# Performance work log

Hardware: AMD Instinct MI355X
Metric: run time of the kernel (lower is better)

The kernel has to match this reference:

```python
import jax, jax.numpy as jnp
import numpy as np

DT = 0.01
T, D_IN, D_STATE = 262144, 64, 128

def setup_inputs() -> dict:
    key = jax.random.key(0)
    k1, k2, k3, k4 = jax.random.split(key, 4)
    U = jax.random.normal(k1, (T, D_IN), dtype=jnp.float32)
    A_log = jax.random.normal(k2, (D_STATE,), dtype=jnp.float32) * 0.1 - 1.0
    B = jax.random.normal(k3, (D_STATE, D_IN), dtype=jnp.float32) * 0.1
    C = jax.random.normal(k4, (D_IN, D_STATE), dtype=jnp.float32) * 0.1
    Dm = jnp.zeros((D_IN, D_IN), dtype=jnp.float32)
    h0 = jnp.zeros((D_STATE,), dtype=jnp.float32)
    return {"U": U, "A_log": A_log, "B": B, "C": C, "D": Dm, "h0": h0}

def reference(U, A_log, B, C, D, h0):
    # Discretized diagonal transition: A_disc = exp(A_log * dt)
    A_d = jnp.exp(A_log * DT)  # (d_state,)
    Bu = U @ B.T               # (T, d_state), precompute all input injections
    Du = U @ D.T               # (T, d_input)

    def step(h, bu):
        h_new = A_d * h + bu
        return h_new, h_new

    h_final, H = jax.lax.scan(step, h0, Bu)  # H: (T, d_state)
    Y = H @ C.T + Du                          # (T, d_input)
    return Y, h_final
```

## Files before the change

### kernel.cpp

```cpp
#include <hip/hip_runtime.h>


#define TT   262144
#define DIN  64
#define DS   128
#define DTC  0.01f
#define L    128
#define NG   (TT / L)
#define SEGL 32
#define NSEG (NG / SEGL)

typedef short  s8v  __attribute__((ext_vector_type(8)));
typedef float  f4v  __attribute__((ext_vector_type(4)));

__device__ __forceinline__ unsigned short f2bf(float f) {
    unsigned u = __float_as_uint(f);
    u += 0x7fffu + ((u >> 16) & 1u);
    return (unsigned short)(u >> 16);
}

__device__ __forceinline__ s8v pack8(float4 a, float4 b) {
    union { unsigned short u[8]; s8v v; } r;
    r.u[0] = f2bf(a.x); r.u[1] = f2bf(a.y); r.u[2] = f2bf(a.z); r.u[3] = f2bf(a.w);
    r.u[4] = f2bf(b.x); r.u[5] = f2bf(b.y); r.u[6] = f2bf(b.z); r.u[7] = f2bf(b.w);
    return r.v;
}

__device__ __forceinline__ int swl(int lane) {
    int q = lane >> 4, m = lane & 15;
    return (q << 4) | (m ^ (q << 2));
}

__device__ __forceinline__ s8v load_bfrag(const float* __restrict__ M,
                                          int row, int k0, int ld) {
    const float4* p = (const float4*)(M + row * ld + k0);
    return pack8(p[0], p[1]);
}

__device__ __forceinline__ void stage_U(const float* __restrict__ Ug,
                                        unsigned short* __restrict__ sA,
                                        int tid) {
    #pragma unroll
    for (int u = tid; u < (L / 16) * 8 * 16; u += 512) {
        int t = u >> 3, oct = u & 7;
        const float4* gp = (const float4*)(Ug + t * 64 + oct * 8);
        float4 x = gp[0], y = gp[1];
        int mt = t >> 4, ks = oct >> 2, q = oct & 3, m = t & 15;
        int slot = (mt * 2 + ks) * 64 + ((q << 4) | (m ^ (q << 2)));
        *(s8v*)&sA[slot * 8] = pack8(x, y);
    }
}

__global__ __launch_bounds__(512) void ssm_k1(
    const float* __restrict__ U, const float* __restrict__ Alog,
    const float* __restrict__ B, float* __restrict__ agg,
    float* __restrict__ segAgg)
{
    __shared__ __align__(16) unsigned short sA[8 * 2 * 64 * 8];
    __shared__ __align__(16) float sBu[64 * 132];
    const int g    = blockIdx.x;
    const int tid  = threadIdx.x;
    const int lane = tid & 63;
    const int w    = tid >> 6;
    const int q    = lane >> 4, m = lane & 15;

    stage_U(U + (size_t)g * L * DIN, sA, tid);

    s8v Bf[2];
    #pragma unroll
    for (int ks = 0; ks < 2; ++ks)
        Bf[ks] = load_bfrag(B, 16 * w + m, ks * 32 + q * 8, DIN);

    float a_s = 0.f, hreg = 0.f;
    if (tid < DS) a_s = __expf(Alog[tid] * DTC);
    __syncthreads();

    #pragma unroll
    for (int hh = 0; hh < 2; ++hh) {
        f4v acc[4];
        #pragma unroll
        for (int mtl = 0; mtl < 4; ++mtl) {
            acc[mtl] = (f4v){0.f, 0.f, 0.f, 0.f};
            const int mt = hh * 4 + mtl;
            #pragma unroll
            for (int ks = 0; ks < 2; ++ks) {
                s8v af = *(const s8v*)&sA[((mt * 2 + ks) * 64 + swl(lane)) * 8];
                acc[mtl] = __builtin_amdgcn_mfma_f32_16x16x32_bf16(af, Bf[ks], acc[mtl], 0, 0, 0);
            }
        }
        #pragma unroll
        for (int mtl = 0; mtl < 4; ++mtl)
            #pragma unroll
            for (int r = 0; r < 4; ++r)
                sBu[(mtl * 16 + q * 4 + r) * 132 + 16 * w + m] = acc[mtl][r];
        __syncthreads();

        if (tid < DS) {
            #pragma unroll
            for (int r = 0; r < 64; ++r)
                hreg = fmaf(a_s, hreg, sBu[r * 132 + tid]);
        }
        __syncthreads();
    }

    if (tid < DS) {
        agg[(size_t)g * DS + tid] = hreg;
        float wgt = __expf(Alog[tid] * (DTC * L) * (float)(SEGL - 1 - (g & (SEGL - 1))));
        atomicAdd(&segAgg[(g >> 5) * DS + tid], hreg * wgt);
    }
}

__global__ void ssm_k2(const float* __restrict__ Alog, const float* __restrict__ h0,
                       const float* __restrict__ segAgg, float* __restrict__ segCarry,
                       float* __restrict__ hfin)
{
    const int s = threadIdx.x;
    const float aSeg = __expf(Alog[s] * (DTC * L * SEGL));
    float c = h0[s];
    #pragma unroll 4
    for (int sg = 0; sg < NSEG; ++sg) {
        segCarry[sg * DS + s] = c;
        c = fmaf(aSeg, c, segAgg[sg * DS + s]);
    }
    hfin[s] = c;
}

__global__ __launch_bounds__(512) void ssm_k3(
    const float* __restrict__ U, const float* __restrict__ Alog,
    const float* __restrict__ B, const float* __restrict__ C,
    const float* __restrict__ Dm, const float* __restrict__ agg,
    const float* __restrict__ segCarry, float* __restrict__ Y)
{
    __shared__ __align__(16) unsigned short sA[8 * 2 * 64 * 8];
    __shared__ __align__(16) float sBu[64 * 132];
    __shared__ __align__(16) unsigned short sH[4 * 4 * 64 * 8];
    const int g    = blockIdx.x;
    const int tid  = threadIdx.x;
    const int lane = tid & 63;
    const int w    = tid >> 6;
    const int q    = lane >> 4, m = lane & 15;

    stage_U(U + (size_t)g * L * DIN, sA, tid);

    s8v Bf[2], Cf[4], Df[2];
    #pragma unroll
    for (int ks = 0; ks < 2; ++ks)
        Bf[ks] = load_bfrag(B, 16 * w + m, ks * 32 + q * 8, DIN);
    const int iC = 16 * (w & 3) + m;
    #pragma unroll
    for (int ks = 0; ks < 4; ++ks)
        Cf[ks] = load_bfrag(C, iC, ks * 32 + q * 8, DS);
    #pragma unroll
    for (int ks = 0; ks < 2; ++ks)
        Df[ks] = load_bfrag(Dm, iC, ks * 32 + q * 8, DIN);

    float a_s = 0.f, hreg = 0.f;
    if (tid < DS) {
        a_s = __expf(Alog[tid] * DTC);
        const float aL = __expf(Alog[tid] * (DTC * L));
        float c0 = segCarry[(g >> 5) * DS + tid];
        for (int c = g & ~(SEGL - 1); c < g; ++c)
            c0 = fmaf(aL, c0, agg[(size_t)c * DS + tid]);
        hreg = c0;
    }
    __syncthreads();

    #pragma unroll
    for (int hh = 0; hh < 2; ++hh) {
        f4v acc[4];
        #pragma unroll
        for (int mtl = 0; mtl < 4; ++mtl) {
            acc[mtl] = (f4v){0.f, 0.f, 0.f, 0.f};
            const int mt = hh * 4 + mtl;
            #pragma unroll
            for (int ks = 0; ks < 2; ++ks) {
                s8v af = *(const s8v*)&sA[((mt * 2 + ks) * 64 + swl(lane)) * 8];
                acc[mtl] = __builtin_amdgcn_mfma_f32_16x16x32_bf16(af, Bf[ks], acc[mtl], 0, 0, 0);
            }
        }
        #pragma unroll
        for (int mtl = 0; mtl < 4; ++mtl)
            #pragma unroll
            for (int r = 0; r < 4; ++r)
                sBu[(mtl * 16 + q * 4 + r) * 132 + 16 * w + m] = acc[mtl][r];
        __syncthreads();

        if (tid < DS) {
            #pragma unroll
            for (int r = 0; r < 64; ++r) {
                hreg = fmaf(a_s, hreg, sBu[r * 132 + tid]);
                sBu[r * 132 + tid] = hreg;
            }
        }
        __syncthreads();

        #pragma unroll
        for (int u = tid; u < 1024; u += 512) {
            int lp = u & 63, ks4 = (u >> 6) & 3, mth = (u >> 8) & 3;
            int qq = (lp >> 4) & 3, mm = lp & 15;
            int t = mth * 16 + mm, s0 = ks4 * 32 + qq * 8;
            const float4* hp = (const float4*)&sBu[t * 132 + s0];
            int slot = (mth * 4 + ks4) * 64 + ((qq << 4) | (mm ^ (qq << 2)));
            *(s8v*)&sH[slot * 8] = pack8(hp[0], hp[1]);
        }
        __syncthreads();

        const int mm2 = w >> 2;
        #pragma unroll
        for (int ti = 0; ti < 2; ++ti) {
            const int mtl = mm2 * 2 + ti;
            f4v acc2 = (f4v){0.f, 0.f, 0.f, 0.f};
            #pragma unroll
            for (int ks = 0; ks < 4; ++ks) {
                s8v ah = *(const s8v*)&sH[((mtl * 4 + ks) * 64 + swl(lane)) * 8];
                acc2 = __builtin_amdgcn_mfma_f32_16x16x32_bf16(ah, Cf[ks], acc2, 0, 0, 0);
            }
            #pragma unroll
            for (int ks = 0; ks < 2; ++ks) {
                s8v au = *(const s8v*)&sA[(((hh * 4 + mtl) * 2 + ks) * 64 + swl(lane)) * 8];
                acc2 = __builtin_amdgcn_mfma_f32_16x16x32_bf16(au, Df[ks], acc2, 0, 0, 0);
            }
            const size_t tb = (size_t)g * L + hh * 64 + mtl * 16 + q * 4;
            #pragma unroll
            for (int r = 0; r < 4; ++r)
                Y[(tb + r) * DIN + iC] = acc2[r];
        }
        __syncthreads();
    }
}

extern "C" void kernel_launch(void* const* d_in, const int* in_sizes, int n_in,
                              void* d_out, int out_size, void* d_ws, size_t ws_size,
                              hipStream_t stream)
{
    const float* U    = (const float*)d_in[0];
    const float* Alog = (const float*)d_in[1];
    const float* B    = (const float*)d_in[2];
    const float* C    = (const float*)d_in[3];
    const float* Dm   = (const float*)d_in[4];
    const float* h0   = (const float*)d_in[5];

    float* out  = (float*)d_out;
    float* Yp   = out;
    float* hfin = out + (size_t)TT * DIN;

    float* agg      = (float*)d_ws;
    float* segAgg   = agg + (size_t)NG * DS;
    float* segCarry = segAgg + (size_t)NSEG * DS;

    hipMemsetAsync(segAgg, 0, (size_t)NSEG * DS * sizeof(float), stream);
    ssm_k1<<<NG, 512, 0, stream>>>(U, Alog, B, agg, segAgg);
    ssm_k2<<<1, DS, 0, stream>>>(Alog, h0, segAgg, segCarry, hfin);
    ssm_k3<<<NG, 512, 0, stream>>>(U, Alog, B, C, Dm, agg, segCarry, Yp);
}
```

Measured before the change: 210.8 us.

## Replace serial chunk scan in pass 1 with decay-weighted MFMA reduction

Pass 1 no longer runs a 128-thread sequential recurrence over the chunk. Each lane now weights its MFMA outputs by the decay power a^(L-1-t) and reduces across lanes with shuffles, which removes the sBu staging buffer and two barriers. Segment length drops from 32 to 16, so the carry walk in pass 3 is shorter, and that walk is rewritten with precomputed decay powers. Pass 3 reuses the sBu storage for the bf16 H tile and adds a ks-dependent XOR swizzle; occupancy hints are added to both kernels. Computing large powers as exp(cA*k) and accumulating weighted sums in a different order may change numerical rounding.

After: 214.3 us. Within noise of the previous version (+1.7%).

```diff
diff --git a/kernel.cpp b/kernel.cpp
--- a/kernel.cpp
+++ b/kernel.cpp
@@ -7,7 +7,7 @@
 #define DTC  0.01f
 #define L    128
 #define NG   (TT / L)
-#define SEGL 32
+#define SEGL 16
 #define NSEG (NG / SEGL)
 
 typedef short  s8v  __attribute__((ext_vector_type(8)));
@@ -26,9 +26,23 @@
     return r.v;
 }
 
-__device__ __forceinline__ int swl(int lane) {
-    int q = lane >> 4, m = lane & 15;
-    return (q << 4) | (m ^ (q << 2));
+__device__ __forceinline__ const s8v* afrag(const unsigned short* sA,
+                                            int mt, int ks, int q, int m) {
+    int slot = (mt * 2 + ks) * 64 + (q << 4) + (m ^ (q << 2) ^ ks);
+    return (const s8v*)&sA[slot * 8];
+}
+
+__device__ __forceinline__ void stage_U(const float* __restrict__ Ug,
+                                        unsigned short* __restrict__ sA,
+                                        int tid) {
+    #pragma unroll
+    for (int p = 0; p < 2; ++p) {
+        int u  = tid + p * 512;
+        int mt = u >> 7, ks = (u >> 6) & 1, q = (u >> 4) & 3, lo = u & 15;
+        int m  = lo ^ (q << 2) ^ ks;
+        const float4* gp = (const float4*)(Ug + (mt * 16 + m) * DIN + ks * 32 + q * 8);
+        *(s8v*)&sA[u * 8] = pack8(gp[0], gp[1]);
+    }
 }
 
 __device__ __forceinline__ s8v load_bfrag(const float* __restrict__ M,
@@ -37,76 +51,51 @@
     return pack8(p[0], p[1]);
 }
 
-__device__ __forceinline__ void stage_U(const float* __restrict__ Ug,
-                                        unsigned short* __restrict__ sA,
-                                        int tid) {
-    #pragma unroll
-    for (int u = tid; u < (L / 16) * 8 * 16; u += 512) {
-        int t = u >> 3, oct = u & 7;
-        const float4* gp = (const float4*)(Ug + t * 64 + oct * 8);
-        float4 x = gp[0], y = gp[1];
-        int mt = t >> 4, ks = oct >> 2, q = oct & 3, m = t & 15;
-        int slot = (mt * 2 + ks) * 64 + ((q << 4) | (m ^ (q << 2)));
-        *(s8v*)&sA[slot * 8] = pack8(x, y);
-    }
-}
-
-__global__ __launch_bounds__(512) void ssm_k1(
+__global__ __launch_bounds__(512, 8) void ssm_k1(
     const float* __restrict__ U, const float* __restrict__ Alog,
     const float* __restrict__ B, float* __restrict__ agg,
     float* __restrict__ segAgg)
 {
-    __shared__ __align__(16) unsigned short sA[8 * 2 * 64 * 8];
-    __shared__ __align__(16) float sBu[64 * 132];
+    __shared__ __align__(16) unsigned short sA[8192];
     const int g    = blockIdx.x;
     const int tid  = threadIdx.x;
     const int lane = tid & 63;
     const int w    = tid >> 6;
     const int q    = lane >> 4, m = lane & 15;
+    const int s    = 16 * w + m;
 
     stage_U(U + (size_t)g * L * DIN, sA, tid);
 
     s8v Bf[2];
     #pragma unroll
     for (int ks = 0; ks < 2; ++ks)
-        Bf[ks] = load_bfrag(B, 16 * w + m, ks * 32 + q * 8, DIN);
-
-    float a_s = 0.f, hreg = 0.f;
-    if (tid < DS) a_s = __expf(Alog[tid] * DTC);
+        Bf[ks] = load_bfrag(B, s, ks * 32 + q * 8, DIN);
+
+    const float cA   = Alog[s] * DTC;
+    const float aInv = __expf(-cA);
     __syncthreads();
 
-    #pragma unroll
-    for (int hh = 0; hh < 2; ++hh) {
-        f4v acc[4];
-        #pragma unroll
-        for (int mtl = 0; mtl < 4; ++mtl) {
-            acc[mtl] = (f4v){0.f, 0.f, 0.f, 0.f};
-            const int mt = hh * 4 + mtl;
-            #pragma unroll
-            for (int ks = 0; ks < 2; ++ks) {
-                s8v af = *(const s8v*)&sA[((mt * 2 + ks) * 64 + swl(lane)) * 8];
-                acc[mtl] = __builtin_amdgcn_mfma_f32_16x16x32_bf16(af, Bf[ks], acc[mtl], 0, 0, 0);
-            }
-        }
-        #pragma unroll
-        for (int mtl = 0; mtl < 4; ++mtl)
-            #pragma unroll
-            for (int r = 0; r < 4; ++r)
-                sBu[(mtl * 16 + q * 4 + r) * 132 + 16 * w + m] = acc[mtl][r];
-        __syncthreads();
-
-        if (tid < DS) {
-            #pragma unroll
-            for (int r = 0; r < 64; ++r)
-                hreg = fmaf(a_s, hreg, sBu[r * 132 + tid]);
-        }
-        __syncthreads();
-    }
-
-    if (tid < DS) {
-        agg[(size_t)g * DS + tid] = hreg;
-        float wgt = __expf(Alog[tid] * (DTC * L) * (float)(SEGL - 1 - (g & (SEGL - 1))));
-        atomicAdd(&segAgg[(g >> 5) * DS + tid], hreg * wgt);
+    float wsum = 0.f;
+    #pragma unroll
+    for (int mt = 0; mt < 8; ++mt) {
+        f4v acc = (f4v){0.f, 0.f, 0.f, 0.f};
+        #pragma unroll
+        for (int ks = 0; ks < 2; ++ks)
+            acc = __builtin_amdgcn_mfma_f32_16x16x32_bf16(*afrag(sA, mt, ks, q, m), Bf[ks], acc, 0, 0, 0);
+        float wb = __expf(cA * (float)(L - 1 - (mt * 16 + q * 4)));
+        #pragma unroll
+        for (int r = 0; r < 4; ++r) {
+            wsum = fmaf(wb, acc[r], wsum);
+            if (r < 3) wb *= aInv;
+        }
+    }
+    wsum += __shfl_xor(wsum, 16, 64);
+    wsum += __shfl_xor(wsum, 32, 64);
+
+    if (q == 0) {
+        agg[(size_t)g * DS + s] = wsum;
+        float wgt = __expf(cA * (float)(L * (SEGL - 1 - (g & (SEGL - 1)))));
+        atomicAdd(&segAgg[(g >> 4) * DS + s], wsum * wgt);
     }
 }
 
@@ -117,7 +106,7 @@
     const int s = threadIdx.x;
     const float aSeg = __expf(Alog[s] * (DTC * L * SEGL));
     float c = h0[s];
-    #pragma unroll 4
+    #pragma unroll 8
     for (int sg = 0; sg < NSEG; ++sg) {
         segCarry[sg * DS + s] = c;
         c = fmaf(aSeg, c, segAgg[sg * DS + s]);
@@ -125,20 +114,22 @@
     hfin[s] = c;
 }
 
-__global__ __launch_bounds__(512) void ssm_k3(
+__global__ __launch_bounds__(512, 6) void ssm_k3(
     const float* __restrict__ U, const float* __restrict__ Alog,
     const float* __restrict__ B, const float* __restrict__ C,
     const float* __restrict__ Dm, const float* __restrict__ agg,
     const float* __restrict__ segCarry, float* __restrict__ Y)
 {
-    __shared__ __align__(16) unsigned short sA[8 * 2 * 64 * 8];
-    __shared__ __align__(16) float sBu[64 * 132];
-    __shared__ __align__(16) unsigned short sH[4 * 4 * 64 * 8];
+    __shared__ __align__(16) unsigned short sA[8192];
+    __shared__ __align__(16) float sBu[64 * 130];
+    unsigned short* sHb = (unsigned short*)sBu;
+
     const int g    = blockIdx.x;
     const int tid  = threadIdx.x;
     const int lane = tid & 63;
     const int w    = tid >> 6;
     const int q    = lane >> 4, m = lane & 15;
+    const int iC   = 16 * (w & 3) + m;
 
     stage_U(U + (size_t)g * L * DIN, sA, tid);
 
@@ -146,7 +137,6 @@
     #pragma unroll
     for (int ks = 0; ks < 2; ++ks)
         Bf[ks] = load_bfrag(B, 16 * w + m, ks * 32 + q * 8, DIN);
-    const int iC = 16 * (w & 3) + m;
     #pragma unroll
     for (int ks = 0; ks < 4; ++ks)
         Cf[ks] = load_bfrag(C, iC, ks * 32 + q * 8, DS);
@@ -156,52 +146,64 @@
 
     float a_s = 0.f, hreg = 0.f;
     if (tid < DS) {
-        a_s = __expf(Alog[tid] * DTC);
-        const float aL = __expf(Alog[tid] * (DTC * L));
-        float c0 = segCarry[(g >> 5) * DS + tid];
-        for (int c = g & ~(SEGL - 1); c < g; ++c)
-            c0 = fmaf(aL, c0, agg[(size_t)c * DS + tid]);
+        const float cA  = Alog[tid] * DTC;
+        a_s = __expf(cA);
+        const float caL = cA * (float)L;
+        const float aL  = __expf(caL);
+        const int   j   = g & (SEGL - 1);
+        const int   gb  = g & ~(SEGL - 1);
+        float c0 = segCarry[(g >> 4) * DS + tid] * __expf(caL * (float)j);
+        float wt = 1.f;
+        for (int c = j - 1; c >= 0; --c) {
+            c0 = fmaf(wt, agg[(size_t)(gb + c) * DS + tid], c0);
+            wt *= aL;
+        }
         hreg = c0;
     }
     __syncthreads();
 
     #pragma unroll
     for (int hh = 0; hh < 2; ++hh) {
-        f4v acc[4];
         #pragma unroll
         for (int mtl = 0; mtl < 4; ++mtl) {
-            acc[mtl] = (f4v){0.f, 0.f, 0.f, 0.f};
+            f4v acc = (f4v){0.f, 0.f, 0.f, 0.f};
             const int mt = hh * 4 + mtl;
             #pragma unroll
-            for (int ks = 0; ks < 2; ++ks) {
-                s8v af = *(const s8v*)&sA[((mt * 2 + ks) * 64 + swl(lane)) * 8];
-                acc[mtl] = __builtin_amdgcn_mfma_f32_16x16x32_bf16(af, Bf[ks], acc[mtl], 0, 0, 0);
+            for (int ks = 0; ks < 2; ++ks)
+                acc = __builtin_amdgcn_mfma_f32_16x16x32_bf16(*afrag(sA, mt, ks, q, m), Bf[ks], acc, 0, 0, 0);
+            #pragma unroll
+            for (int r = 0; r < 4; ++r)
+                sBu[(mtl * 16 + q * 4 + r) * 130 + 16 * w + m] = acc[r];
+        }
+        __syncthreads();
+
+        if (tid < DS) {
+            #pragma unroll
+            for (int r = 0; r < 64; ++r) {
+                hreg = fmaf(a_s, hreg, sBu[r * 130 + tid]);
+                sBu[r * 130 + tid] = hreg;
             }
         }
-        #pragma unroll
-        for (int mtl = 0; mtl < 4; ++mtl)
-            #pragma unroll
-            for (int r = 0; r < 4; ++r)
-                sBu[(mtl * 16 + q * 4 + r) * 132 + 16 * w + m] = acc[mtl][r];
-        __syncthreads();
-
-        if (tid < DS) {
-            #pragma unroll
-            for (int r = 0; r < 64; ++r) {
-                hreg = fmaf(a_s, hreg, sBu[r * 132 + tid]);
-                sBu[r * 132 + tid] = hreg;
-            }
-        }
-        __syncthreads();
-
-        #pragma unroll
-        for (int u = tid; u < 1024; u += 512) {
-            int lp = u & 63, ks4 = (u >> 6) & 3, mth = (u >> 8) & 3;
-            int qq = (lp >> 4) & 3, mm = lp & 15;
-            int t = mth * 16 + mm, s0 = ks4 * 32 + qq * 8;
-            const float4* hp = (const float4*)&sBu[t * 132 + s0];
-            int slot = (mth * 4 + ks4) * 64 + ((qq << 4) | (mm ^ (qq << 2)));
-            *(s8v*)&sH[slot * 8] = pack8(hp[0], hp[1]);
+        __syncthreads();
+
+        float4 pr[2][2];
+        int tt[2], cc[2];
+        #pragma unroll
+        for (int p = 0; p < 2; ++p) {
+            int u  = tid + p * 512;
+            int t  = (u & 3) + ((u >> 6) << 2);
+            int c8 = (u >> 2) & 15;
+            tt[p] = t; cc[p] = c8;
+            const float4* hp = (const float4*)&sBu[t * 130 + c8 * 8];
+            pr[p][0] = hp[0]; pr[p][1] = hp[1];
+        }
+        __syncthreads();
+        #pragma unroll
+        for (int p = 0; p < 2; ++p) {
+            int t = tt[p], c8 = cc[p];
+            int mth = t >> 4, mm = t & 15, ks4 = c8 >> 2, qq = c8 & 3;
+            int slot = mth * 256 + ks4 * 64 + qq * 16 + (mm ^ (qq << 2) ^ ks4);
+            *(s8v*)&sHb[slot * 8] = pack8(pr[p][0], pr[p][1]);
         }
         __syncthreads();
 
@@ -212,14 +214,12 @@
             f4v acc2 = (f4v){0.f, 0.f, 0.f, 0.f};
             #pragma unroll
             for (int ks = 0; ks < 4; ++ks) {
-                s8v ah = *(const s8v*)&sH[((mtl * 4 + ks) * 64 + swl(lane)) * 8];
-                acc2 = __builtin_amdgcn_mfma_f32_16x16x32_bf16(ah, Cf[ks], acc2, 0, 0, 0);
+                int slot = mtl * 256 + ks * 64 + q * 16 + (m ^ (q << 2) ^ ks);
+                acc2 = __builtin_amdgcn_mfma_f32_16x16x32_bf16(*(const s8v*)&sHb[slot * 8], Cf[ks], acc2, 0, 0, 0);
             }
             #pragma unroll
-            for (int ks = 0; ks < 2; ++ks) {
-                s8v au = *(const s8v*)&sA[(((hh * 4 + mtl) * 2 + ks) * 64 + swl(lane)) * 8];
-                acc2 = __builtin_amdgcn_mfma_f32_16x16x32_bf16(au, Df[ks], acc2, 0, 0, 0);
-            }
+            for (int ks = 0; ks < 2; ++ks)
+                acc2 = __builtin_amdgcn_mfma_f32_16x16x32_bf16(*afrag(sA, hh * 4 + mtl, ks, q, m), Df[ks], acc2, 0, 0, 0);
             const size_t tb = (size_t)g * L + hh * 64 + mtl * 16 + q * 4;
             #pragma unroll
             for (int r = 0; r < 4; ++r)
```
